# Optimization experiments

Hardware: AMD Instinct MI355X
Metric: run time of the kernel (lower is better)

The kernel has to match this reference:

```python
import jax, jax.numpy as jnp
import numpy as np

DIM = 1024
N_HEADS = 16
N_KV_HEADS = 4
HEAD_DIM = DIM // N_HEADS  # 64
N_EXPERTS = 8
TOP_K = 2
ROPE_BASE = 10000.0


def setup_inputs() -> dict:
    key = jax.random.key(0)
    ks = jax.random.split(key, 12)
    B, L, D = 2, 1024, DIM
    s = lambda *sh: 0.02
    inp = {
        "x": jax.random.normal(ks[0], (B, L, D), jnp.float32),
        # attention projections (stored [in, out])
        "wq": jax.random.normal(ks[1], (D, D), jnp.float32) * 0.02,
        "wk": jax.random.normal(ks[2], (D, N_KV_HEADS * HEAD_DIM), jnp.float32) * 0.02,
        "wv": jax.random.normal(ks[3], (D, N_KV_HEADS * HEAD_DIM), jnp.float32) * 0.02,
        "wo": jax.random.normal(ks[4], (D, D), jnp.float32) * 0.02,
        # MoE router + stacked expert FFN weights
        "wg": jax.random.normal(ks[5], (D, N_EXPERTS), jnp.float32) * 0.02,
        "w1": jax.random.normal(ks[6], (N_EXPERTS, D, 4 * D), jnp.float32) * 0.02,
        "w2": jax.random.normal(ks[7], (N_EXPERTS, 4 * D, D), jnp.float32) * 0.02,
        # pre-attention / pre-MoE LayerNorms
        "ln1_g": jnp.ones((D,), jnp.float32),
        "ln1_b": jnp.zeros((D,), jnp.float32),
        "ln2_g": jnp.ones((D,), jnp.float32),
        "ln2_b": jnp.zeros((D,), jnp.float32),
    }
    return inp


def _layernorm(x, g, b, eps=1e-5):
    mu = x.mean(-1, keepdims=True)
    var = ((x - mu) ** 2).mean(-1, keepdims=True)
    return (x - mu) * jax.lax.rsqrt(var + eps) * g + b


def _rope_cos_sin(L, dtype):
    inv_freq = 1.0 / (ROPE_BASE ** (jnp.arange(0, HEAD_DIM, 2, dtype=jnp.float32) / HEAD_DIM))
    t = jnp.arange(L, dtype=jnp.float32)
    freqs = jnp.einsum('i,j->ij', t, inv_freq)          # [L, hd/2]
    emb = jnp.concatenate([freqs, freqs], axis=-1)       # [L, hd]
    return jnp.cos(emb).astype(dtype), jnp.sin(emb).astype(dtype)


def _rotate_half(x):
    x1, x2 = jnp.split(x, 2, axis=-1)
    return jnp.concatenate([-x2, x1], axis=-1)


def _attention(h, wq, wk, wv, wo):
    B, L, D = h.shape
    q = (h @ wq).reshape(B, L, N_HEADS, HEAD_DIM).transpose(0, 2, 1, 3)      # [B,H,L,hd]
    k = (h @ wk).reshape(B, L, N_KV_HEADS, HEAD_DIM).transpose(0, 2, 1, 3)   # [B,Hkv,L,hd]
    v = (h @ wv).reshape(B, L, N_KV_HEADS, HEAD_DIM).transpose(0, 2, 1, 3)
    cos, sin = _rope_cos_sin(L, h.dtype)                  # [L,hd] each
    cos = cos[None, None]; sin = sin[None, None]
    q = q * cos + _rotate_half(q) * sin
    k = k * cos + _rotate_half(k) * sin
    n_rep = N_HEADS // N_KV_HEADS
    k = jnp.repeat(k, n_rep, axis=1)                      # repeat_interleave over head dim
    v = jnp.repeat(v, n_rep, axis=1)
    scores = jnp.einsum('bhqd,bhkd->bhqk', q, k) / jnp.sqrt(jnp.asarray(HEAD_DIM, h.dtype))
    causal = jnp.tril(jnp.ones((L, L), bool))
    scores = jnp.where(causal[None, None], scores, jnp.finfo(scores.dtype).min)
    attn = jax.nn.softmax(scores, axis=-1)
    out = jnp.einsum('bhqk,bhkd->bhqd', attn, v).transpose(0, 2, 1, 3).reshape(B, L, D)
    return out @ wo


def _moe(h, wg, w1, w2):
    B, L, D = h.shape
    gate_logits = h @ wg                                  # [B,L,E]
    top_v, top_i = jax.lax.top_k(gate_logits, TOP_K)      # [B,L,K]
    gates = jax.nn.softmax(top_v, axis=-1)                # [B,L,K]
    one_hot = jax.nn.one_hot(top_i, N_EXPERTS, dtype=h.dtype)   # [B,L,K,E]
    comb = jnp.einsum('blke,blk->ble', one_hot, gates)    # per-token per-expert weight
    # naive MoE: every expert processes every token (as in the source loop)
    hid = jax.nn.gelu(jnp.einsum('bld,edf->eblf', h, w1), approximate=False)  # [E,B,L,4D]
    eout = jnp.einsum('eblf,efd->ebld', hid, w2)          # [E,B,L,D]
    out = jnp.einsum('ebld,ble->bld', eout, comb)
    # load-balance loss from expert assignment counts (buffer starts at zero)
    counts = one_hot.sum(axis=(0, 1, 2))                  # [E]
    counts_norm = counts / counts.sum()
    lb_loss = jnp.mean((counts_norm - 1.0 / N_EXPERTS) ** 2)
    return out, lb_loss


def reference(x, wq, wk, wv, wo, wg, w1, w2, ln1_g, ln1_b, ln2_g, ln2_b):
    h = _layernorm(x, ln1_g, ln1_b)
    x = x + _attention(h, wq, wk, wv, wo)
    h = _layernorm(x, ln2_g, ln2_b)
    moe_out, lb_loss = _moe(h, wg, w1, w2)
    x = x + moe_out
    return x, lb_loss
```

## Files before the change

### kernel.cpp

```cpp
#include <hip/hip_runtime.h>
#include <hip/hip_bf16.h>

#define NTOK   2048
#define DMODEL 1024
#define NEXP   8
#define DFF    4096
#define MAXROWS 5120
#define MAXTILES 40

typedef __attribute__((ext_vector_type(8))) short short8;
typedef __attribute__((ext_vector_type(4))) float float4v;

__device__ __forceinline__ unsigned short f2bf(float f) {
  union { float f; unsigned u; } v; v.f = f;
  unsigned r = v.u + 0x7fffu + ((v.u >> 16) & 1u);
  return (unsigned short)(r >> 16);
}
__device__ __forceinline__ float bf2f(unsigned short h) {
  union { unsigned u; float f; } v; v.u = ((unsigned)h) << 16; return v.f;
}
__device__ __forceinline__ void gl_lds16(const void* g, void* l) {
  __builtin_amdgcn_global_load_lds((const __attribute__((address_space(1))) void*)g,
                                   (__attribute__((address_space(3))) void*)l, 16, 0, 0);
}

template<int EPI, int EMAP>
__launch_bounds__(256, 2)
__global__ void gemm_bt(const unsigned short* __restrict__ A,
                        const unsigned short* __restrict__ B0,
                        float* __restrict__ C,
                        unsigned short* __restrict__ Cbf,
                        const int N, const int K,
                        const int* __restrict__ tmap, const long estride) {
  const int mtile = blockIdx.y;
  const unsigned short* B = B0;
  if (EMAP) {
    int e = tmap[mtile];
    if (e < 0) return;
    B += (size_t)e * (size_t)estride;
  }
  const int n0 = blockIdx.x * 128;
  const int m0 = mtile * 128;
  __shared__ unsigned short sA[128 * 64];
  __shared__ unsigned short sB[128 * 64];
  const int tid  = threadIdx.x;
  const int w    = tid >> 6;
  const int lane = tid & 63;
  const int quad = lane >> 4;
  const int r16  = lane & 15;
  const int wr   = w >> 1;
  const int wc   = w & 1;
  const int rl   = lane >> 3;
  const int csl  = lane & 7;
  const int cg   = csl ^ rl;
  float4v acc[4][4];
#pragma unroll
  for (int i = 0; i < 4; ++i)
#pragma unroll
    for (int j = 0; j < 4; ++j) acc[i][j] = float4v{0.f, 0.f, 0.f, 0.f};

  const unsigned short* Ab = A + (size_t)m0 * K + cg * 8;
  const unsigned short* Bb = B + (size_t)n0 * K + cg * 8;

  for (int k0 = 0; k0 < K; k0 += 64) {
    __syncthreads();
#pragma unroll
    for (int i = 0; i < 4; ++i) {
      const int j = w * 4 + i;
      gl_lds16(Ab + (size_t)(j * 8 + rl) * K + k0, (char*)sA + j * 1024);
      gl_lds16(Bb + (size_t)(j * 8 + rl) * K + k0, (char*)sB + j * 1024);
    }
    __syncthreads();
#pragma unroll
    for (int kc = 0; kc < 8; kc += 4) {
      short8 af[4], bq[4];
#pragma unroll
      for (int mt = 0; mt < 4; ++mt) {
        int r = wr * 64 + mt * 16 + r16;
        af[mt] = *(const short8*)(sA + ((r * 8 + ((kc + quad) ^ (r & 7))) * 8));
      }
#pragma unroll
      for (int nt = 0; nt < 4; ++nt) {
        int r = wc * 64 + nt * 16 + r16;
        bq[nt] = *(const short8*)(sB + ((r * 8 + ((kc + quad) ^ (r & 7))) * 8));
      }
#pragma unroll
      for (int mt = 0; mt < 4; ++mt)
#pragma unroll
        for (int nt = 0; nt < 4; ++nt)
          acc[mt][nt] = __builtin_amdgcn_mfma_f32_16x16x32_bf16(af[mt], bq[nt], acc[mt][nt], 0, 0, 0);
    }
  }
#pragma unroll
  for (int mt = 0; mt < 4; ++mt) {
#pragma unroll
    for (int nt = 0; nt < 4; ++nt) {
#pragma unroll
      for (int rg = 0; rg < 4; ++rg) {
        const int m = m0 + wr * 64 + mt * 16 + quad * 4 + rg;
        const int n = n0 + wc * 64 + nt * 16 + r16;
        const size_t idx = (size_t)m * N + n;
        const float v = acc[mt][nt][rg];
        if (EPI == 0) C[idx] = v;
        else {
          float ge = 0.5f * v * (1.0f + erff(v * 0.70710678118654752440f));
          Cbf[idx] = f2bf(ge);
        }
      }
    }
  }
}

template<int EPI>
__launch_bounds__(256, 2)
__global__ void gemm_split(const unsigned short* __restrict__ Ah,
                           const unsigned short* __restrict__ Al,
                           const unsigned short* __restrict__ Bh,
                           const unsigned short* __restrict__ Bl,
                           float* __restrict__ C, const float* __restrict__ R,
                           const int N, const int K) {
  const int n0 = blockIdx.x * 128;
  const int m0 = blockIdx.y * 128;
  __shared__ unsigned short sAh[128 * 64];
  __shared__ unsigned short sAl[128 * 64];
  __shared__ unsigned short sBh[128 * 64];
  __shared__ unsigned short sBl[128 * 64];
  const int tid  = threadIdx.x;
  const int w    = tid >> 6;
  const int lane = tid & 63;
  const int quad = lane >> 4;
  const int r16  = lane & 15;
  const int wr   = w >> 1;
  const int wc   = w & 1;
  const int rl   = lane >> 3;
  const int csl  = lane & 7;
  const int cg   = csl ^ rl;
  float4v acc[4][4];
#pragma unroll
  for (int i = 0; i < 4; ++i)
#pragma unroll
    for (int j = 0; j < 4; ++j) acc[i][j] = float4v{0.f, 0.f, 0.f, 0.f};

  const size_t aoff = (size_t)m0 * K + cg * 8;
  const size_t boff = (size_t)n0 * K + cg * 8;

  for (int k0 = 0; k0 < K; k0 += 64) {
    __syncthreads();
#pragma unroll
    for (int i = 0; i < 4; ++i) {
      const int j = w * 4 + i;
      const size_t ro = (size_t)(j * 8 + rl) * K + k0;
      gl_lds16(Ah + aoff + ro, (char*)sAh + j * 1024);
      gl_lds16(Al + aoff + ro, (char*)sAl + j * 1024);
      gl_lds16(Bh + boff + ro, (char*)sBh + j * 1024);
      gl_lds16(Bl + boff + ro, (char*)sBl + j * 1024);
    }
    __syncthreads();
#pragma unroll
    for (int kc = 0; kc < 8; kc += 4) {
      short8 afh[4], afl[4], bqh[4], bql[4];
#pragma unroll
      for (int mt = 0; mt < 4; ++mt) {
        int r = wr * 64 + mt * 16 + r16;
        int o = (r * 8 + ((kc + quad) ^ (r & 7))) * 8;
        afh[mt] = *(const short8*)(sAh + o);
        afl[mt] = *(const short8*)(sAl + o);
      }
#pragma unroll
      for (int nt = 0; nt < 4; ++nt) {
        int r = wc * 64 + nt * 16 + r16;
        int o = (r * 8 + ((kc + quad) ^ (r & 7))) * 8;
        bqh[nt] = *(const short8*)(sBh + o);
        bql[nt] = *(const short8*)(sBl + o);
      }
#pragma unroll
      for (int mt = 0; mt < 4; ++mt)
#pragma unroll
        for (int nt = 0; nt < 4; ++nt) {
          acc[mt][nt] = __builtin_amdgcn_mfma_f32_16x16x32_bf16(afh[mt], bqh[nt], acc[mt][nt], 0, 0, 0);
          acc[mt][nt] = __builtin_amdgcn_mfma_f32_16x16x32_bf16(afh[mt], bql[nt], acc[mt][nt], 0, 0, 0);
          acc[mt][nt] = __builtin_amdgcn_mfma_f32_16x16x32_bf16(afl[mt], bqh[nt], acc[mt][nt], 0, 0, 0);
        }
    }
  }
#pragma unroll
  for (int mt = 0; mt < 4; ++mt) {
#pragma unroll
    for (int nt = 0; nt < 4; ++nt) {
#pragma unroll
      for (int rg = 0; rg < 4; ++rg) {
        const int m = m0 + wr * 64 + mt * 16 + quad * 4 + rg;
        const int n = n0 + wc * 64 + nt * 16 + r16;
        const size_t idx = (size_t)m * N + n;
        const float v = acc[mt][nt][rg];
        if (EPI == 0) C[idx] = v;
        else C[idx] = v + R[idx];
      }
    }
  }
}

template<int WLO>
__global__ void transpose_w(const float* __restrict__ in, unsigned short* __restrict__ oh,
                            unsigned short* __restrict__ ol, const int K, const int N,
                            const long istride, const long ostride) {
  const int bz = blockIdx.z;
  in += (size_t)bz * istride;
  oh += (size_t)bz * ostride;
  if (WLO) ol += (size_t)bz * ostride;
  __shared__ float t[32][33];
  const int n0 = blockIdx.x * 32;
  const int k0 = blockIdx.y * 32;
  const int tx = threadIdx.x;
  const int ty = threadIdx.y;
#pragma unroll
  for (int i = 0; i < 4; ++i)
    t[ty + i * 8][tx] = in[(size_t)(k0 + ty + i * 8) * N + n0 + tx];
  __syncthreads();
#pragma unroll
  for (int i = 0; i < 4; ++i) {
    float v = t[tx][ty + i * 8];
    size_t o = (size_t)(n0 + ty + i * 8) * K + k0 + tx;
    unsigned short h = f2bf(v);
    oh[o] = h;
    if (WLO) ol[o] = f2bf(v - bf2f(h));
  }
}

__global__ void ln_kernel(const float* __restrict__ x, const float* __restrict__ g,
                          const float* __restrict__ b, unsigned short* __restrict__ hi,
                          unsigned short* __restrict__ lo, float* __restrict__ f32o) {
  const int row = blockIdx.x;
  const int tid = threadIdx.x;
  const int w = tid >> 6, lane = tid & 63;
  const float4 v = *(const float4*)(x + (size_t)row * DMODEL + tid * 4);
  float s = v.x + v.y + v.z + v.w;
  float q = v.x * v.x + v.y * v.y + v.z * v.z + v.w * v.w;
#pragma unroll
  for (int o = 32; o; o >>= 1) { s += __shfl_xor(s, o); q += __shfl_xor(q, o); }
  __shared__ float red[8];
  if (lane == 0) { red[w] = s; red[4 + w] = q; }
  __syncthreads();
  s = red[0] + red[1] + red[2] + red[3];
  q = red[4] + red[5] + red[6] + red[7];
  const float mean = s * (1.0f / DMODEL);
  const float var = q * (1.0f / DMODEL) - mean * mean;
  const float rs = rsqrtf(var + 1e-5f);
  const float4 gg = *(const float4*)(g + tid * 4);
  const float4 bb = *(const float4*)(b + tid * 4);
  float y[4];
  y[0] = (v.x - mean) * rs * gg.x + bb.x;
  y[1] = (v.y - mean) * rs * gg.y + bb.y;
  y[2] = (v.z - mean) * rs * gg.z + bb.z;
  y[3] = (v.w - mean) * rs * gg.w + bb.w;
  const size_t base = (size_t)row * DMODEL + tid * 4;
#pragma unroll
  for (int i = 0; i < 4; ++i) {
    unsigned short h = f2bf(y[i]);
    hi[base + i] = h;
    if (lo) lo[base + i] = f2bf(y[i] - bf2f(h));
    if (f32o) f32o[base + i] = y[i];
  }
}

__global__ void rope_split(const float* __restrict__ qkv,
                           unsigned short* __restrict__ q_hi, unsigned short* __restrict__ q_lo,
                           unsigned short* __restrict__ k_hi, unsigned short* __restrict__ k_lo) {
  const int rowtok = blockIdx.x;
  const int b = rowtok >> 10;
  const int l = rowtok & 1023;
  const int tid = threadIdx.x;
  __shared__ float cb[32], sb[32];
  if (tid < 32) {
    float inv = powf(10000.0f, -(float)tid * (1.0f / 32.0f));
    float ang = (float)l * inv;
    cb[tid] = cosf(ang);
    sb[tid] = sinf(ang);
  }
  __syncthreads();
  const float* src = qkv + (size_t)rowtok * 1536;
#pragma unroll
  for (int it = 0; it < 5; ++it) {
    const int e = tid + it * 256;
    const int hh = e >> 6;
    const int d = e & 63;
    const int dm = d & 31;
    float val = src[e];
    float partner = (d < 32) ? -src[e + 32] : src[e - 32];
    float ov = val * cb[dm] + partner * sb[dm];
    unsigned short hv = f2bf(ov);
    unsigned short lv = f2bf(ov - bf2f(hv));
    if (hh < 16) {
      size_t idx = ((size_t)(b * 16 + hh) * 1024 + l) * 64 + d;
      q_hi[idx] = hv; q_lo[idx] = lv;
    } else {
      size_t idx = ((size_t)(b * 4 + (hh - 16)) * 1024 + l) * 64 + d;
      k_hi[idx] = hv; k_lo[idx] = lv;
    }
  }
}

__global__ void vt_split(const float* __restrict__ qkv,
                         unsigned short* __restrict__ vt_hi, unsigned short* __restrict__ vt_lo) {
  const int bkvh = blockIdx.z;
  const int b = bkvh >> 2;
  const int kvh = bkvh & 3;
  const float* src = qkv + (size_t)b * 1024 * 1536 + 1280 + kvh * 64;
  __shared__ float t[32][33];
  const int l0 = blockIdx.y * 32;
  const int d0 = blockIdx.x * 32;
  const int tx = threadIdx.x;
  const int ty = threadIdx.y;
#pragma unroll
  for (int i = 0; i < 4; ++i)
    t[ty + i * 8][tx] = src[(size_t)(l0 + ty + i * 8) * 1536 + d0 + tx];
  __syncthreads();
#pragma unroll
  for (int i = 0; i < 4; ++i) {
    float v = t[tx][ty + i * 8];
    size_t o = (size_t)bkvh * 65536 + (size_t)(d0 + ty + i * 8) * 1024 + l0 + tx;
    unsigned short h = f2bf(v);
    vt_hi[o] = h;
    vt_lo[o] = f2bf(v - bf2f(h));
  }
}

__launch_bounds__(256, 2)
__global__ void attn_mfma(const unsigned short* __restrict__ q_hi, const unsigned short* __restrict__ q_lo,
                          const unsigned short* __restrict__ k_hi, const unsigned short* __restrict__ k_lo,
                          const unsigned short* __restrict__ vt_hi, const unsigned short* __restrict__ vt_lo,
                          unsigned short* __restrict__ ohi, unsigned short* __restrict__ olo) {
  const int blk = blockIdx.x;
  const int bh = blk & 31;
  const int qt = 15 - (blk >> 5);
  const int b = bh >> 4;
  const int h = bh & 15;
  const int kvbh = b * 4 + (h >> 2);
  const int q0 = qt * 64;
  const int tid = threadIdx.x;
  const int w = tid >> 6;
  const int lane = tid & 63;
  const int quad = lane >> 4;
  const int r16 = lane & 15;
  const int rl = lane >> 3;
  const int csl = lane & 7;
  const int cg = csl ^ rl;

  __shared__ unsigned short sK[2][64 * 64];
  __shared__ unsigned short sV[2][64 * 64];
  __shared__ unsigned short sP[2][64 * 64];

  short8 qfh[2], qfl[2];
  {
    const size_t qrow = ((size_t)bh * 1024 + q0 + w * 16 + r16) * 64 + quad * 8;
    qfh[0] = *(const short8*)(q_hi + qrow);
    qfh[1] = *(const short8*)(q_hi + qrow + 32);
    qfl[0] = *(const short8*)(q_lo + qrow);
    qfl[1] = *(const short8*)(q_lo + qrow + 32);
  }
  float4v O[4];
#pragma unroll
  for (int nt = 0; nt < 4; ++nt) O[nt] = float4v{0.f, 0.f, 0.f, 0.f};
  float m[4], l[4];
#pragma unroll
  for (int rg = 0; rg < 4; ++rg) { m[rg] = -__builtin_inff(); l[rg] = 0.f; }

  const unsigned short* khb = k_hi + (size_t)kvbh * 65536 + cg * 8;
  const unsigned short* klb = k_lo + (size_t)kvbh * 65536 + cg * 8;
  const unsigned short* vhb = vt_hi + (size_t)kvbh * 65536 + cg * 8;
  const unsigned short* vlb = vt_lo + (size_t)kvbh * 65536 + cg * 8;

  for (int c = 0; c <= qt; ++c) {
    __syncthreads();
#pragma unroll
    for (int j = 0; j < 2; ++j) {
      const int i = w * 2 + j;
      const int row = i * 8 + rl;
      gl_lds16(khb + (size_t)(c * 64 + row) * 64, (char*)sK[0] + i * 1024);
      gl_lds16(klb + (size_t)(c * 64 + row) * 64, (char*)sK[1] + i * 1024);
      gl_lds16(vhb + (size_t)row * 1024 + c * 64, (char*)sV[0] + i * 1024);
      gl_lds16(vlb + (size_t)row * 1024 + c * 64, (char*)sV[1] + i * 1024);
    }
    __syncthreads();

    float4v S[4];
#pragma unroll
    for (int nt = 0; nt < 4; ++nt) S[nt] = float4v{0.f, 0.f, 0.f, 0.f};
#pragma unroll
    for (int ks = 0; ks < 2; ++ks) {
#pragma unroll
      for (int nt = 0; nt < 4; ++nt) {
        const int r = nt * 16 + r16;
        const int o = (r * 8 + ((ks * 4 + quad) ^ (r & 7))) * 8;
        const short8 kh = *(const short8*)(sK[0] + o);
        const short8 kl = *(const short8*)(sK[1] + o);
        S[nt] = __builtin_amdgcn_mfma_f32_16x16x32_bf16(qfh[ks], kh, S[nt], 0, 0, 0);
        S[nt] = __builtin_amdgcn_mfma_f32_16x16x32_bf16(qfh[ks], kl, S[nt], 0, 0, 0);
        S[nt] = __builtin_amdgcn_mfma_f32_16x16x32_bf16(qfl[ks], kh, S[nt], 0, 0, 0);
      }
    }
    const float NEGINF = -__builtin_inff();
#pragma unroll
    for (int nt = 0; nt < 4; ++nt)
#pragma unroll
      for (int rg = 0; rg < 4; ++rg) S[nt][rg] *= 0.125f;
    if (c == qt) {
#pragma unroll
      for (int nt = 0; nt < 4; ++nt) {
        const int col = nt * 16 + r16;
#pragma unroll
        for (int rg = 0; rg < 4; ++rg) {
          const int row = w * 16 + quad * 4 + rg;
          if (col > row) S[nt][rg] = NEGINF;
        }
      }
    }
    float alpha[4], lsum[4];
#pragma unroll
    for (int rg = 0; rg < 4; ++rg) {
      float mx = fmaxf(fmaxf(S[0][rg], S[1][rg]), fmaxf(S[2][rg], S[3][rg]));
      mx = fmaxf(mx, __shfl_xor(mx, 1));
      mx = fmaxf(mx, __shfl_xor(mx, 2));
      mx = fmaxf(mx, __shfl_xor(mx, 4));
      mx = fmaxf(mx, __shfl_xor(mx, 8));
      const float mn = fmaxf(m[rg], mx);
      alpha[rg] = __expf(m[rg] - mn);
      m[rg] = mn;
      lsum[rg] = 0.f;
    }
#pragma unroll
    for (int nt = 0; nt < 4; ++nt)
#pragma unroll
      for (int rg = 0; rg < 4; ++rg) {
        const float e = __expf(S[nt][rg] - m[rg]);
        S[nt][rg] = e;
        lsum[rg] += e;
      }
#pragma unroll
    for (int rg = 0; rg < 4; ++rg) {
      float ls = lsum[rg];
      ls += __shfl_xor(ls, 1);
      ls += __shfl_xor(ls, 2);
      ls += __shfl_xor(ls, 4);
      ls += __shfl_xor(ls, 8);
      l[rg] = l[rg] * alpha[rg] + ls;
    }
#pragma unroll
    for (int nt = 0; nt < 4; ++nt) {
      const int key = nt * 16 + r16;
      const int chunk = key >> 3;
#pragma unroll
      for (int rg = 0; rg < 4; ++rg) {
        const int r = w * 16 + quad * 4 + rg;
        const int addr = r * 64 + ((chunk ^ (r & 7)) * 8) + (key & 7);
        const float e = S[nt][rg];
        const unsigned short hv = f2bf(e);
        sP[0][addr] = hv;
        sP[1][addr] = f2bf(e - bf2f(hv));
      }
    }
#pragma unroll
    for (int nt = 0; nt < 4; ++nt)
#pragma unroll
      for (int rg = 0; rg < 4; ++rg) O[nt][rg] *= alpha[rg];
#pragma unroll
    for (int ks = 0; ks < 2; ++ks) {
      const int rA = w * 16 + r16;
      const int oA = (rA * 8 + ((ks * 4 + quad) ^ (rA & 7))) * 8;
      const short8 ph = *(const short8*)(sP[0] + oA);
      const short8 pl = *(const short8*)(sP[1] + oA);
#pragma unroll
      for (int nt = 0; nt < 4; ++nt) {
        const int rv = nt * 16 + r16;
        const int ov = (rv * 8 + ((ks * 4 + quad) ^ (rv & 7))) * 8;
        const short8 vh = *(const short8*)(sV[0] + ov);
        const short8 vl = *(const short8*)(sV[1] + ov);
        O[nt] = __builtin_amdgcn_mfma_f32_16x16x32_bf16(ph, vh, O[nt], 0, 0, 0);
        O[nt] = __builtin_amdgcn_mfma_f32_16x16x32_bf16(ph, vl, O[nt], 0, 0, 0);
        O[nt] = __builtin_amdgcn_mfma_f32_16x16x32_bf16(pl, vh, O[nt], 0, 0, 0);
      }
    }
  }
#pragma unroll
  for (int nt = 0; nt < 4; ++nt) {
    const int col = h * 64 + nt * 16 + r16;
#pragma unroll
    for (int rg = 0; rg < 4; ++rg) {
      const int row = q0 + w * 16 + quad * 4 + rg;
      const float ovv = O[nt][rg] / l[rg];
      const size_t idx = ((size_t)b * 1024 + row) * DMODEL + col;
      const unsigned short hv = f2bf(ovv);
      ohi[idx] = hv;
      olo[idx] = f2bf(ovv - bf2f(hv));
    }
  }
}

#define RED6SUM(X) { X += __shfl_xor(X,32); X += __shfl_xor(X,16); X += __shfl_xor(X,8); X += __shfl_xor(X,4); X += __shfl_xor(X,2); X += __shfl_xor(X,1); }

__global__ void router_kernel(const float* __restrict__ h2f, const float* __restrict__ wg,
                              int* __restrict__ tok_e, float* __restrict__ tok_g,
                              int* __restrict__ counts) {
  const int t = blockIdx.x;
  const int lane = threadIdx.x;
  float acc[8] = {0,0,0,0,0,0,0,0};
  const float* hr = h2f + (size_t)t * DMODEL;
  for (int d = lane; d < DMODEL; d += 64) {
    const float hv = hr[d];
    const float4 w0 = *(const float4*)(wg + d * 8);
    const float4 w1_ = *(const float4*)(wg + d * 8 + 4);
    acc[0] += hv * w0.x; acc[1] += hv * w0.y; acc[2] += hv * w0.z; acc[3] += hv * w0.w;
    acc[4] += hv * w1_.x; acc[5] += hv * w1_.y; acc[6] += hv * w1_.z; acc[7] += hv * w1_.w;
  }
#pragma unroll
  for (int e = 0; e < 8; ++e) { RED6SUM(acc[e]); }
  if (lane == 0) {
    int i0 = 0; float v0 = acc[0];
#pragma unroll
    for (int e = 1; e < 8; ++e) if (acc[e] > v0) { v0 = acc[e]; i0 = e; }
    int i1 = -1; float v1 = -__builtin_inff();
#pragma unroll
    for (int e = 0; e < 8; ++e) if (e != i0 && acc[e] > v1) { v1 = acc[e]; i1 = e; }
    const float ex = __expf(v1 - v0);
    const float den = 1.0f + ex;
    tok_e[t * 2] = i0; tok_e[t * 2 + 1] = i1;
    tok_g[t * 2] = 1.0f / den; tok_g[t * 2 + 1] = ex / den;
    atomicAdd(counts + i0, 1);
    atomicAdd(counts + i1, 1);
  }
}

__global__ void finalize_kernel(const int* __restrict__ counts, int* __restrict__ off_pad,
                                int* __restrict__ tile_map, float* __restrict__ lb_out) {
  if (threadIdx.x == 0 && blockIdx.x == 0) {
    int tile = 0, rowoff = 0;
    for (int e = 0; e < NEXP; ++e) {
      off_pad[e] = rowoff;
      const int c = counts[e];
      const int nt = (c + 127) >> 7;
      for (int i = 0; i < nt; ++i) tile_map[tile++] = e;
      rowoff += nt * 128;
    }
    for (; tile < MAXTILES; ++tile) tile_map[tile] = -1;
    float sacc = 0.f;
    for (int e = 0; e < NEXP; ++e) {
      const float cn = (float)counts[e] * (1.0f / 4096.0f);
      const float d = cn - 0.125f;
      sacc += d * d;
    }
    lb_out[0] = sacc * (1.0f / 8.0f);
  }
}

__global__ void scatter_kernel(const int* __restrict__ tok_e, const int* __restrict__ off_pad,
                               int* __restrict__ fill, int* __restrict__ tok_pos,
                               const unsigned short* __restrict__ h2bf, unsigned short* __restrict__ Xg) {
  const int slot = blockIdx.x;
  const int t = slot >> 1;
  __shared__ int sp;
  if (threadIdx.x == 0) {
    const int e = tok_e[slot];
    const int r = atomicAdd(fill + e, 1);
    const int ppos = off_pad[e] + r;
    tok_pos[slot] = ppos;
    sp = ppos;
  }
  __syncthreads();
  const int pos = sp;
  *(uint2*)(Xg + (size_t)pos * DMODEL + threadIdx.x * 4) =
      *(const uint2*)(h2bf + (size_t)t * DMODEL + threadIdx.x * 4);
}

__global__ void combine_kernel(const float* __restrict__ x1, const float* __restrict__ eout,
                               const int* __restrict__ tok_pos, const float* __restrict__ tok_g,
                               float* __restrict__ out) {
  const int t = blockIdx.x;
  const int tid = threadIdx.x;
  const int p0 = tok_pos[t * 2], p1 = tok_pos[t * 2 + 1];
  const float g0 = tok_g[t * 2], g1 = tok_g[t * 2 + 1];
  const size_t o = (size_t)t * DMODEL + tid * 4;
  const float4 a = *(const float4*)(x1 + o);
  const float4 e0 = *(const float4*)(eout + (size_t)p0 * DMODEL + tid * 4);
  const float4 e1 = *(const float4*)(eout + (size_t)p1 * DMODEL + tid * 4);
  float4 r;
  r.x = a.x + g0 * e0.x + g1 * e1.x;
  r.y = a.y + g0 * e0.y + g1 * e1.y;
  r.z = a.z + g0 * e0.z + g1 * e1.z;
  r.w = a.w + g0 * e0.w + g1 * e1.w;
  *(float4*)(out + o) = r;
}

__global__ void init_kernel(int* counts, int* fill) {
  const int t = threadIdx.x;
  if (t < 8) { counts[t] = 0; fill[t] = 0; }
}

extern "C" void kernel_launch(void* const* d_in, const int* in_sizes, int n_in,
                              void* d_out, int out_size, void* d_ws, size_t ws_size,
                              hipStream_t stream) {
  (void)in_sizes; (void)n_in; (void)out_size; (void)ws_size;
  const float* x    = (const float*)d_in[0];
  const float* wq   = (const float*)d_in[1];
  const float* wk   = (const float*)d_in[2];
  const float* wv   = (const float*)d_in[3];
  const float* wo   = (const float*)d_in[4];
  const float* wg   = (const float*)d_in[5];
  const float* w1   = (const float*)d_in[6];
  const float* w2   = (const float*)d_in[7];
  const float* ln1g = (const float*)d_in[8];
  const float* ln1b = (const float*)d_in[9];
  const float* ln2g = (const float*)d_in[10];
  const float* ln2b = (const float*)d_in[11];
  float* out = (float*)d_out;

  char* p = (char*)d_ws;
  auto take = [&](size_t n) { void* r = (void*)p; p += (n + 255) & ~(size_t)255; return r; };
  unsigned short* h1_hi   = (unsigned short*)take((size_t)NTOK * DMODEL * 2);
  unsigned short* h1_lo   = (unsigned short*)take((size_t)NTOK * DMODEL * 2);
  unsigned short* wqkv_hi = (unsigned short*)take((size_t)1536 * 1024 * 2);
  unsigned short* wqkv_lo = (unsigned short*)take((size_t)1536 * 1024 * 2);
  unsigned short* woT_hi  = (unsigned short*)take((size_t)1024 * 1024 * 2);
  unsigned short* woT_lo  = (unsigned short*)take((size_t)1024 * 1024 * 2);
  unsigned short* w1t     = (unsigned short*)take((size_t)NEXP * DFF * DMODEL * 2);
  unsigned short* w2t     = (unsigned short*)take((size_t)NEXP * DMODEL * DFF * 2);
  float* qkv   = (float*)take((size_t)NTOK * 1536 * 4);
  unsigned short* q_hi  = (unsigned short*)take((size_t)2 * 16 * 1024 * 64 * 2);
  unsigned short* q_lo  = (unsigned short*)take((size_t)2 * 16 * 1024 * 64 * 2);
  unsigned short* k_hi  = (unsigned short*)take((size_t)2 * 4 * 1024 * 64 * 2);
  unsigned short* k_lo  = (unsigned short*)take((size_t)2 * 4 * 1024 * 64 * 2);
  unsigned short* vt_hi = (unsigned short*)take((size_t)2 * 4 * 1024 * 64 * 2);
  unsigned short* vt_lo = (unsigned short*)take((size_t)2 * 4 * 1024 * 64 * 2);
  unsigned short* attn_hi = (unsigned short*)take((size_t)NTOK * DMODEL * 2);
  unsigned short* attn_lo = (unsigned short*)take((size_t)NTOK * DMODEL * 2);
  float* x1    = (float*)take((size_t)NTOK * DMODEL * 4);
  float* h2f   = (float*)take((size_t)NTOK * DMODEL * 4);
  unsigned short* h2bf = (unsigned short*)take((size_t)NTOK * DMODEL * 2);
  unsigned short* Xg   = (unsigned short*)take((size_t)MAXROWS * DMODEL * 2);
  unsigned short* hid  = (unsigned short*)take((size_t)MAXROWS * DFF * 2);
  float* eout  = (float*)take((size_t)MAXROWS * DMODEL * 4);
  int*   tok_e   = (int*)take(4096 * 4);
  float* tok_g   = (float*)take(4096 * 4);
  int*   tok_pos = (int*)take(4096 * 4);
  int*   counts  = (int*)take(64);
  int*   fill    = (int*)take(64);
  int*   off_pad = (int*)take(64);
  int*   tile_map = (int*)take(256);

  init_kernel<<<1, 64, 0, stream>>>(counts, fill);
  ln_kernel<<<NTOK, 256, 0, stream>>>(x, ln1g, ln1b, h1_hi, h1_lo, nullptr);
  transpose_w<1><<<dim3(32, 32, 1), dim3(32, 8), 0, stream>>>(wq, wqkv_hi, wqkv_lo, 1024, 1024, 0, 0);
  transpose_w<1><<<dim3(8, 32, 1), dim3(32, 8), 0, stream>>>(wk, wqkv_hi + (size_t)1024 * 1024, wqkv_lo + (size_t)1024 * 1024, 1024, 256, 0, 0);
  transpose_w<1><<<dim3(8, 32, 1), dim3(32, 8), 0, stream>>>(wv, wqkv_hi + (size_t)1280 * 1024, wqkv_lo + (size_t)1280 * 1024, 1024, 256, 0, 0);
  transpose_w<1><<<dim3(32, 32, 1), dim3(32, 8), 0, stream>>>(wo, woT_hi, woT_lo, 1024, 1024, 0, 0);
  transpose_w<0><<<dim3(128, 32, 8), dim3(32, 8), 0, stream>>>(w1, w1t, nullptr, 1024, 4096, (long)1024 * 4096, (long)4096 * 1024);
  transpose_w<0><<<dim3(32, 128, 8), dim3(32, 8), 0, stream>>>(w2, w2t, nullptr, 4096, 1024, (long)4096 * 1024, (long)1024 * 4096);
  gemm_split<0><<<dim3(12, 16), 256, 0, stream>>>(h1_hi, h1_lo, wqkv_hi, wqkv_lo, qkv, nullptr, 1536, 1024);
  rope_split<<<NTOK, 256, 0, stream>>>(qkv, q_hi, q_lo, k_hi, k_lo);
  vt_split<<<dim3(2, 32, 8), dim3(32, 8), 0, stream>>>(qkv, vt_hi, vt_lo);
  attn_mfma<<<512, 256, 0, stream>>>(q_hi, q_lo, k_hi, k_lo, vt_hi, vt_lo, attn_hi, attn_lo);
  gemm_split<2><<<dim3(8, 16), 256, 0, stream>>>(attn_hi, attn_lo, woT_hi, woT_lo, x1, x, 1024, 1024);
  ln_kernel<<<NTOK, 256, 0, stream>>>(x1, ln2g, ln2b, h2bf, nullptr, h2f);
  router_kernel<<<NTOK, 64, 0, stream>>>(h2f, wg, tok_e, tok_g, counts);
  finalize_kernel<<<1, 64, 0, stream>>>(counts, off_pad, tile_map, out + (size_t)NTOK * DMODEL);
  scatter_kernel<<<4096, 256, 0, stream>>>(tok_e, off_pad, fill, tok_pos, h2bf, Xg);
  gemm_bt<3,1><<<dim3(32, MAXTILES), 256, 0, stream>>>(Xg, w1t, nullptr, hid, DFF, DMODEL, tile_map, (long)DFF * DMODEL);
  gemm_bt<0,1><<<dim3(8, MAXTILES), 256, 0, stream>>>(hid, w2t, eout, nullptr, DMODEL, DFF, tile_map, (long)DMODEL * DFF);
  combine_kernel<<<NTOK, 256, 0, stream>>>(x1, eout, tok_pos, tok_g, out);
}
```

Baseline: 758.1 us.

## Vectorize weight transpose with 64x64 tiles and raise gemm_bt occupancy hint

The weight transpose/convert kernel now uses 64x64 tiles with float4 global loads and ushort4 packed bf16 stores instead of 32x32 tiles with scalar accesses. This targets the memory-bound conversion of the large w1/w2 expert weights, which move about 256 MB of fp32 per call. Separately, gemm_bt's launch bounds change from 2 to 4 blocks per CU, which may force register pressure or spills in the expert GEMMs. The LDS tile grows to about 16.6 KB per block.

Result: no change. 755.0 us (-0.4%).

```diff
diff --git a/kernel.cpp b/kernel.cpp
--- a/kernel.cpp
+++ b/kernel.cpp
@@ -25,7 +25,7 @@
 }
 
 template<int EPI, int EMAP>
-__launch_bounds__(256, 2)
+__launch_bounds__(256, 4)
 __global__ void gemm_bt(const unsigned short* __restrict__ A,
                         const unsigned short* __restrict__ B0,
                         float* __restrict__ C,
@@ -208,22 +208,37 @@
   in += (size_t)bz * istride;
   oh += (size_t)bz * ostride;
   if (WLO) ol += (size_t)bz * ostride;
-  __shared__ float t[32][33];
-  const int n0 = blockIdx.x * 32;
-  const int k0 = blockIdx.y * 32;
-  const int tx = threadIdx.x;
-  const int ty = threadIdx.y;
-#pragma unroll
-  for (int i = 0; i < 4; ++i)
-    t[ty + i * 8][tx] = in[(size_t)(k0 + ty + i * 8) * N + n0 + tx];
+  __shared__ float t[64][65];
+  const int n0 = blockIdx.x * 64;
+  const int k0 = blockIdx.y * 64;
+  const int tid = threadIdx.x;
+  const int rr = tid >> 4;
+  const int c4 = (tid & 15) * 4;
+#pragma unroll
+  for (int p = 0; p < 4; ++p) {
+    const int row = p * 16 + rr;
+    const float4 v = *(const float4*)(in + (size_t)(k0 + row) * N + n0 + c4);
+    t[row][c4] = v.x; t[row][c4 + 1] = v.y; t[row][c4 + 2] = v.z; t[row][c4 + 3] = v.w;
+  }
   __syncthreads();
 #pragma unroll
-  for (int i = 0; i < 4; ++i) {
-    float v = t[tx][ty + i * 8];
-    size_t o = (size_t)(n0 + ty + i * 8) * K + k0 + tx;
-    unsigned short h = f2bf(v);
-    oh[o] = h;
-    if (WLO) ol[o] = f2bf(v - bf2f(h));
+  for (int p = 0; p < 4; ++p) {
+    const int n = p * 16 + rr;
+    float vs[4];
+#pragma unroll
+    for (int i = 0; i < 4; ++i) vs[i] = t[c4 + i][n];
+    ushort4 h;
+    h.x = f2bf(vs[0]); h.y = f2bf(vs[1]); h.z = f2bf(vs[2]); h.w = f2bf(vs[3]);
+    const size_t o = (size_t)(n0 + n) * K + k0 + c4;
+    *(ushort4*)(oh + o) = h;
+    if (WLO) {
+      ushort4 lo4;
+      lo4.x = f2bf(vs[0] - bf2f(h.x));
+      lo4.y = f2bf(vs[1] - bf2f(h.y));
+      lo4.z = f2bf(vs[2] - bf2f(h.z));
+      lo4.w = f2bf(vs[3] - bf2f(h.w));
+      *(ushort4*)(ol + o) = lo4;
+    }
   }
 }
 
@@ -648,12 +663,12 @@
 
   init_kernel<<<1, 64, 0, stream>>>(counts, fill);
   ln_kernel<<<NTOK, 256, 0, stream>>>(x, ln1g, ln1b, h1_hi, h1_lo, nullptr);
-  transpose_w<1><<<dim3(32, 32, 1), dim3(32, 8), 0, stream>>>(wq, wqkv_hi, wqkv_lo, 1024, 1024, 0, 0);
-  transpose_w<1><<<dim3(8, 32, 1), dim3(32, 8), 0, stream>>>(wk, wqkv_hi + (size_t)1024 * 1024, wqkv_lo + (size_t)1024 * 1024, 1024, 256, 0, 0);
-  transpose_w<1><<<dim3(8, 32, 1), dim3(32, 8), 0, stream>>>(wv, wqkv_hi + (size_t)1280 * 1024, wqkv_lo + (size_t)1280 * 1024, 1024, 256, 0, 0);
-  transpose_w<1><<<dim3(32, 32, 1), dim3(32, 8), 0, stream>>>(wo, woT_hi, woT_lo, 1024, 1024, 0, 0);
-  transpose_w<0><<<dim3(128, 32, 8), dim3(32, 8), 0, stream>>>(w1, w1t, nullptr, 1024, 4096, (long)1024 * 4096, (long)4096 * 1024);
-  transpose_w<0><<<dim3(32, 128, 8), dim3(32, 8), 0, stream>>>(w2, w2t, nullptr, 4096, 1024, (long)4096 * 1024, (long)1024 * 4096);
+  transpose_w<1><<<dim3(16, 16, 1), 256, 0, stream>>>(wq, wqkv_hi, wqkv_lo, 1024, 1024, 0, 0);
+  transpose_w<1><<<dim3(4, 16, 1), 256, 0, stream>>>(wk, wqkv_hi + (size_t)1024 * 1024, wqkv_lo + (size_t)1024 * 1024, 1024, 256, 0, 0);
+  transpose_w<1><<<dim3(4, 16, 1), 256, 0, stream>>>(wv, wqkv_hi + (size_t)1280 * 1024, wqkv_lo + (size_t)1280 * 1024, 1024, 256, 0, 0);
+  transpose_w<1><<<dim3(16, 16, 1), 256, 0, stream>>>(wo, woT_hi, woT_lo, 1024, 1024, 0, 0);
+  transpose_w<0><<<dim3(64, 16, 8), 256, 0, stream>>>(w1, w1t, nullptr, 1024, 4096, (long)1024 * 4096, (long)4096 * 1024);
+  transpose_w<0><<<dim3(16, 64, 8), 256, 0, stream>>>(w2, w2t, nullptr, 4096, 1024, (long)4096 * 1024, (long)1024 * 4096);
   gemm_split<0><<<dim3(12, 16), 256, 0, stream>>>(h1_hi, h1_lo, wqkv_hi, wqkv_lo, qkv, nullptr, 1536, 1024);
   rope_split<<<NTOK, 256, 0, stream>>>(qkv, q_hi, q_lo, k_hi, k_lo);
   vt_split<<<dim3(2, 32, 8), dim3(32, 8), 0, stream>>>(qkv, vt_hi, vt_lo);
```
